# Optimization experiments

Hardware: AMD Instinct MI355X
Metric: run time of the kernel (lower is better)

The kernel has to match this reference:

```python
import jax, jax.numpy as jnp
import numpy as np

EPS = 1e-5
RADIUS = 3.0
NSAMPLE = 32


def _bn(x, g, b, axes):
    # BatchNorm (training-mode batch statistics) over given axes; channel is axis 1.
    m = jnp.mean(x, axis=axes, keepdims=True)
    v = jnp.var(x, axis=axes, keepdims=True)
    shape = [1, -1] + [1] * (x.ndim - 2)
    return (x - m) / jnp.sqrt(v + EPS) * g.reshape(shape) + b.reshape(shape)


def _ball_query(xyz, new_xyz, radius, nsample):
    # xyz: (B,N,3) support points, new_xyz: (B,M,3) query points -> idx (B,M,nsample) int32
    # Matches pointnet2 ball_query: first `nsample` points within radius (in index order),
    # padded with the first found index (0 if none found).
    d2 = (jnp.sum(new_xyz ** 2, -1)[:, :, None]
          + jnp.sum(xyz ** 2, -1)[:, None, :]
          - 2.0 * jnp.einsum('bmd,bnd->bmn', new_xyz, xyz))  # (B,M,N)
    mask = d2 < radius * radius
    N = xyz.shape[1]
    scores = jnp.where(mask, -jnp.arange(N, dtype=d2.dtype), -jnp.inf)
    vals, _ = jax.lax.top_k(scores, nsample)  # largest scores = smallest indices, in order
    valid = jnp.isfinite(vals)
    idx = jnp.where(valid, -vals, 0.0).astype(jnp.int32)
    first = idx[..., 0:1]
    return jnp.where(valid, idx, first)


def setup_inputs() -> dict:
    key = jax.random.key(0)
    ks = jax.random.split(key, 8)
    B, N, M, C = 4, 16384, 2048, 128
    inp = {
        'ffps_xyz': jax.random.normal(ks[0], (B, M, 3), jnp.float32),
        'backbone_xyz': jax.random.normal(ks[1], (B, N, 3), jnp.float32),
        'backbone_features': jax.random.normal(ks[2], (B, C, N), jnp.float32),
        'shift_w0': jax.random.normal(ks[3], (64, 3), jnp.float32) * 0.1,
        'shift_g0': jnp.ones((64,), jnp.float32),
        'shift_b0': jnp.zeros((64,), jnp.float32),
        'shift_w1': jax.random.normal(ks[4], (3, 64), jnp.float32) * 0.1,
        'shift_g1': jnp.ones((3,), jnp.float32),
        'shift_b1': jnp.zeros((3,), jnp.float32),
        'mlp_w0': jax.random.normal(ks[5], (128, 131), jnp.float32) * 0.05,
        'mlp_g0': jnp.ones((128,), jnp.float32),
        'mlp_b0': jnp.zeros((128,), jnp.float32),
        'mlp_w1': jax.random.normal(ks[6], (256, 128), jnp.float32) * 0.05,
        'mlp_g1': jnp.ones((256,), jnp.float32),
        'mlp_b1': jnp.zeros((256,), jnp.float32),
    }
    return inp


def reference(ffps_xyz, backbone_xyz, backbone_features,
              shift_w0, shift_g0, shift_b0, shift_w1, shift_g1, shift_b1,
              mlp_w0, mlp_g0, mlp_b0, mlp_w1, mlp_g1, mlp_b1):
    # shift_layer: Conv1d(1x1)+BN1d+ReLU stack on candidate coordinates
    q = ffps_xyz.transpose(0, 2, 1)  # (B,3,M)
    h = jax.nn.relu(_bn(jnp.einsum('oc,bcm->bom', shift_w0, q), shift_g0, shift_b0, (0, 2)))
    h = jax.nn.relu(_bn(jnp.einsum('oc,bcm->bom', shift_w1, h), shift_g1, shift_b1, (0, 2)))
    new_xyz = h.transpose(0, 2, 1)  # (B,M,3) shifted candidate centers

    # QueryAndGroup(use_xyz=True)
    idx = _ball_query(backbone_xyz, new_xyz, RADIUS, NSAMPLE)        # (B,M,K)
    grouped_xyz = jax.vmap(lambda x, i: x[i])(backbone_xyz, idx)      # (B,M,K,3)
    grouped_feat = jax.vmap(lambda f, i: f[:, i])(backbone_features, idx)  # (B,C,M,K)
    rel = (grouped_xyz - new_xyz[:, :, None, :]).transpose(0, 3, 1, 2)     # (B,3,M,K)
    g = jnp.concatenate([rel, grouped_feat], axis=1)                  # (B,3+C,M,K)

    # Conv2d(1x1)+BN2d+ReLU stack
    g = jax.nn.relu(_bn(jnp.einsum('oc,bcmk->bomk', mlp_w0, g), mlp_g0, mlp_b0, (0, 2, 3)))
    g = jax.nn.relu(_bn(jnp.einsum('oc,bcmk->bomk', mlp_w1, g), mlp_g1, mlp_b1, (0, 2, 3)))

    # max-pool over neighbor dim, squeeze, transpose -> (B,M,C_out)
    out = jnp.max(g, axis=3)  # (B,C_out,M)
    return out.transpose(0, 2, 1)
```

## Files before the change

### kernel.cpp

```cpp
#include <hip/hip_runtime.h>
#include <cstddef>
#include <cstdint>

#define B_ 4
#define N_ 16384
#define M_ 2048
#define C_ 128
#define NQ (B_*M_)
#define NSAMP 32
#define SAMP (NQ*NSAMP)
#define EPS_ 1e-5f
#define R2_ 9.0f

typedef short s8v  __attribute__((ext_vector_type(8)));
typedef short s4v  __attribute__((ext_vector_type(4)));
typedef float f32x4 __attribute__((ext_vector_type(4)));

#define ST_COPIES 8
#define ST_S0S 0
#define ST_S0Q 64
#define ST_S1S 128
#define ST_S1Q 136
#define ST_M1S 144
#define ST_M1Q 272
#define ST_M2S 400
#define ST_M2Q 656

__device__ __forceinline__ unsigned short f2bf(float f) {
    unsigned int u = __builtin_bit_cast(unsigned int, f);
    u += 0x7fffu + ((u >> 16) & 1u);
    return (unsigned short)(u >> 16);
}
__device__ __forceinline__ float bf2f(unsigned short h) {
    unsigned int u = ((unsigned int)h) << 16;
    return __builtin_bit_cast(float, u);
}

__global__ void k_prep_w(const float* __restrict__ w0, const float* __restrict__ w1,
                         unsigned short* __restrict__ w0p, unsigned short* __restrict__ w1p) {
    int i = blockIdx.x * 256 + threadIdx.x;
    const int tot0 = 128 * 160;
    if (i < tot0) {
        int o = i / 160, c = i - o * 160;
        float v = 0.f;
        if (c < 128)      v = w0[o * 131 + 3 + c];
        else if (c < 131) v = w0[o * 131 + (c - 128)];
        w0p[i] = f2bf(v);
    }
    int j = i - tot0;
    if (j >= 0 && j < 256 * 128) w1p[j] = f2bf(w1[j]);
}

__global__ void k_transpose(const float* __restrict__ feat, unsigned short* __restrict__ featT) {
    __shared__ unsigned short tl[64][130];
    int b  = blockIdx.x >> 8;
    int n0 = (blockIdx.x & 255) * 64;
    const float* src = feat + (size_t)b * C_ * N_;
    int t = threadIdx.x;
    for (int i = 0; i < 32; ++i) {
        int lin = i * 256 + t;
        int c = lin >> 6, n = lin & 63;
        tl[n][c] = f2bf(src[(size_t)c * N_ + n0 + n]);
    }
    __syncthreads();
    unsigned short* dst = featT + ((size_t)b * N_ + n0) * 128;
    #pragma unroll
    for (int i = 0; i < 4; ++i) {
        int lin = i * 256 + t;
        int n = lin >> 4, cg = lin & 15;
        s8v v;
        #pragma unroll
        for (int e = 0; e < 8; ++e) v[e] = (short)tl[n][cg*8 + e];
        *(s8v*)(dst + (size_t)n * 128 + cg * 8) = v;
    }
}

__global__ void k_shift0(const float* __restrict__ xyz, const float* __restrict__ w0s,
                         float* __restrict__ t0, float* __restrict__ stats) {
    __shared__ float w[192];
    __shared__ float ps[4][64], pq[4][64];
    int t = threadIdx.x, wave = t >> 6, lane = t & 63;
    if (t < 192) w[t] = w0s[t];
    __syncthreads();
    int p = blockIdx.x * 256 + t;
    float q0 = xyz[p*3], q1 = xyz[p*3+1], q2 = xyz[p*3+2];
    float* orow = t0 + (size_t)p * 64;
    #pragma unroll
    for (int o = 0; o < 64; ++o) {
        float v = w[3*o]*q0 + w[3*o+1]*q1 + w[3*o+2]*q2;
        orow[o] = v;
        float s = v, sq = v * v;
        #pragma unroll
        for (int mk = 32; mk; mk >>= 1) { s += __shfl_xor(s, mk); sq += __shfl_xor(sq, mk); }
        if (lane == 0) { ps[wave][o] = s; pq[wave][o] = sq; }
    }
    __syncthreads();
    if (t < 64) {
        float s = ps[0][t] + ps[1][t] + ps[2][t] + ps[3][t];
        float q = pq[0][t] + pq[1][t] + pq[2][t] + pq[3][t];
        atomicAdd(&stats[ST_S0S + t], s);
        atomicAdd(&stats[ST_S0Q + t], q);
    }
}

__global__ void k_shift1(const float* __restrict__ t0, const float* __restrict__ w1s,
                         const float* __restrict__ g0, const float* __restrict__ b0,
                         float* __restrict__ t1, float* __restrict__ stats) {
    __shared__ float aa[64], bb[64], wl[192];
    __shared__ float ps[4][3], pq[4][3];
    int t = threadIdx.x, wave = t >> 6, lane = t & 63;
    if (t < 64) {
        float mean = stats[ST_S0S + t] * (1.f / NQ);
        float var  = stats[ST_S0Q + t] * (1.f / NQ) - mean * mean;
        float a = g0[t] * rsqrtf(var + EPS_);
        aa[t] = a; bb[t] = b0[t] - mean * a;
    }
    if (t < 192) wl[t] = w1s[t];
    __syncthreads();
    int p = blockIdx.x * 256 + t;
    const f32x4* xr = (const f32x4*)(t0 + (size_t)p * 64);
    float v0 = 0.f, v1 = 0.f, v2 = 0.f;
    #pragma unroll
    for (int i = 0; i < 16; ++i) {
        f32x4 x = xr[i];
        #pragma unroll
        for (int j = 0; j < 4; ++j) {
            int c = 4*i + j;
            float h = fmaxf(0.f, aa[c] * x[j] + bb[c]);
            v0 += wl[c] * h; v1 += wl[64 + c] * h; v2 += wl[128 + c] * h;
        }
    }
    t1[p*3] = v0; t1[p*3+1] = v1; t1[p*3+2] = v2;
    float vv[3] = {v0, v1, v2};
    #pragma unroll
    for (int o = 0; o < 3; ++o) {
        float s = vv[o], q = vv[o] * vv[o];
        #pragma unroll
        for (int mk = 32; mk; mk >>= 1) { s += __shfl_xor(s, mk); q += __shfl_xor(q, mk); }
        if (lane == 0) { ps[wave][o] = s; pq[wave][o] = q; }
    }
    __syncthreads();
    if (t < 3) {
        float s = ps[0][t] + ps[1][t] + ps[2][t] + ps[3][t];
        float q = pq[0][t] + pq[1][t] + pq[2][t] + pq[3][t];
        atomicAdd(&stats[ST_S1S + t], s);
        atomicAdd(&stats[ST_S1Q + t], q);
    }
}

__global__ void k_shift2(const float* __restrict__ t1, const float* __restrict__ g1,
                         const float* __restrict__ b1, const float* __restrict__ stats,
                         float* __restrict__ nxyz) {
    int p = blockIdx.x * 256 + threadIdx.x;
    for (int o = 0; o < 3; ++o) {
        float mean = stats[ST_S1S + o] * (1.f / NQ);
        float var  = stats[ST_S1Q + o] * (1.f / NQ) - mean * mean;
        float a = g1[o] * rsqrtf(var + EPS_);
        float bbv = b1[o] - mean * a;
        nxyz[p*3+o] = fmaxf(0.f, a * t1[p*3+o] + bbv);
    }
}

__global__ void __launch_bounds__(256)
k_ballq(const float* __restrict__ bxyz, const float* __restrict__ nxyz,
        int* __restrict__ idxb) {
    __shared__ float pts[4096 * 3];
    int tid = threadIdx.x, wave = tid >> 6, lane = tid & 63;
    int b = blockIdx.x >> 5;
    int qbase = blockIdx.x * 64 + wave * 16;
    const float* bp = bxyz + (size_t)b * N_ * 3;
    unsigned long long below = (lane == 63) ? ~0ull >> 1 : ((1ull << lane) - 1ull);

    float qx[16], qy[16], qz[16], sq[16];
    int cnt[16], first[16];
    #pragma unroll
    for (int q = 0; q < 16; ++q) {
        qx[q] = nxyz[(qbase+q)*3]; qy[q] = nxyz[(qbase+q)*3+1]; qz[q] = nxyz[(qbase+q)*3+2];
        sq[q] = __fadd_rn(__fadd_rn(__fmul_rn(qx[q],qx[q]), __fmul_rn(qy[q],qy[q])), __fmul_rn(qz[q],qz[q]));
        cnt[q] = 0; first[q] = 0;
    }

    for (int ch = 0; ch < 4; ++ch) {
        __syncthreads();
        {
            const f32x4* src = (const f32x4*)(bp + ch * 12288);
            f32x4* d4 = (f32x4*)pts;
            #pragma unroll
            for (int i = 0; i < 12; ++i) d4[i*256 + tid] = src[i*256 + tid];
        }
        __syncthreads();
        #pragma unroll
        for (int q = 0; q < 16; ++q) {
            if (cnt[q] >= 32) continue;
            for (int j0 = 0; j0 < 4096 && cnt[q] < 32; j0 += 256) {
                #pragma unroll
                for (int u = 0; u < 4; ++u) {
                    if (cnt[q] < 32) {
                        int jl = j0 + u*64 + lane;
                        float x = pts[jl*3], y = pts[jl*3+1], z = pts[jl*3+2];
                        float sx  = __fadd_rn(__fadd_rn(__fmul_rn(x,x), __fmul_rn(y,y)), __fmul_rn(z,z));
                        float dot = __fadd_rn(__fadd_rn(__fmul_rn(qx[q],x), __fmul_rn(qy[q],y)), __fmul_rn(qz[q],z));
                        float d2  = __fsub_rn(__fadd_rn(sq[q], sx), __fmul_rn(2.0f, dot));
                        unsigned long long m = __ballot(d2 < R2_);
                        if (cnt[q] == 0 && m != 0ull)
                            first[q] = ch*4096 + j0 + u*64 + __ffsll((long long)m) - 1;
                        int pre = cnt[q] + __popcll(m & below);
                        if (((m >> lane) & 1ull) && pre < 32)
                            idxb[(size_t)(qbase+q)*32 + pre] = ch*4096 + jl;
                        cnt[q] += __popcll(m);
                    }
                }
            }
        }
    }
    #pragma unroll
    for (int q = 0; q < 16; ++q) {
        if (cnt[q] < 32) {
            int f = (cnt[q] == 0) ? 0 : first[q];
            for (int k = cnt[q] + lane; k < 32; k += 64) idxb[(size_t)(qbase+q)*32 + k] = f;
        }
    }
}

__global__ void __launch_bounds__(256)
k_gemm1(const unsigned short* __restrict__ featT, const float* __restrict__ bxyz,
        const float* __restrict__ nxyz, const int* __restrict__ idxb,
        const unsigned short* __restrict__ w0p, unsigned short* __restrict__ y1,
        float* __restrict__ stats) {
    __shared__ unsigned short gt[64][168];
    __shared__ int pidx[256];
    __shared__ float nq[8][3];
    int tid  = threadIdx.x;
    int wave = tid >> 6, lane = tid & 63, quad = lane >> 4, l16 = lane & 15;
    int s2 = tid >> 2, part4 = tid & 3;
    int b = blockIdx.x >> 8;
    float* stc = stats + (size_t)(blockIdx.x & (ST_COPIES-1)) * 1024;

    s8v bfr[2][5];
    #pragma unroll
    for (int g = 0; g < 2; ++g)
        #pragma unroll
        for (int kk = 0; kk < 5; ++kk)
            bfr[g][kk] = *(const s8v*)(w0p + (wave*32 + g*16 + l16)*160 + kk*32 + quad*8);

    pidx[tid] = idxb[blockIdx.x * 256 + tid];
    if (tid < 24) nq[tid / 3][tid % 3] = nxyz[blockIdx.x * 24 + tid];
    if (tid < 64)
        for (int c = 131; c < 160; ++c) gt[tid][c] = 0;
    __syncthreads();

    s8v pv[4]; float prel0 = 0.f, prel1 = 0.f, prel2 = 0.f;
    {
        int pp = pidx[s2];
        const unsigned short* src = featT + ((size_t)(b * N_ + pp)) * 128 + part4 * 32;
        pv[0] = *(const s8v*)src;        pv[1] = *(const s8v*)(src + 8);
        pv[2] = *(const s8v*)(src + 16); pv[3] = *(const s8v*)(src + 24);
        if (tid < 64) {
            int pq_ = pidx[tid];
            const float* bx = bxyz + (size_t)(b * N_ + pq_) * 3;
            int q = tid >> 5;
            prel0 = bx[0] - nq[q][0]; prel1 = bx[1] - nq[q][1]; prel2 = bx[2] - nq[q][2];
        }
    }
    float csum[2] = {}, csq[2] = {};

    for (int r = 0; r < 4; ++r) {
        __syncthreads();
        *(s8v*)&gt[s2][part4*32]      = pv[0];
        *(s8v*)&gt[s2][part4*32 + 8]  = pv[1];
        *(s8v*)&gt[s2][part4*32 + 16] = pv[2];
        *(s8v*)&gt[s2][part4*32 + 24] = pv[3];
        if (tid < 64) {
            gt[tid][128] = f2bf(prel0); gt[tid][129] = f2bf(prel1); gt[tid][130] = f2bf(prel2);
        }
        if (r + 1 < 4) {
            int pp = pidx[(r+1)*64 + s2];
            const unsigned short* src = featT + ((size_t)(b * N_ + pp)) * 128 + part4 * 32;
            pv[0] = *(const s8v*)src;        pv[1] = *(const s8v*)(src + 8);
            pv[2] = *(const s8v*)(src + 16); pv[3] = *(const s8v*)(src + 24);
            if (tid < 64) {
                int pq_ = pidx[(r+1)*64 + tid];
                const float* bx = bxyz + (size_t)(b * N_ + pq_) * 3;
                int q = (r+1)*2 + (tid >> 5);
                prel0 = bx[0] - nq[q][0]; prel1 = bx[1] - nq[q][1]; prel2 = bx[2] - nq[q][2];
            }
        }
        __syncthreads();
        f32x4 acc[2][4] = {};
        #pragma unroll
        for (int kk = 0; kk < 5; ++kk) {
            s8v at[4];
            #pragma unroll
            for (int t = 0; t < 4; ++t)
                at[t] = *(const s8v*)&gt[t*16 + l16][kk*32 + quad*8];
            #pragma unroll
            for (int g = 0; g < 2; ++g)
                #pragma unroll
                for (int t = 0; t < 4; ++t)
                    acc[g][t] = __builtin_amdgcn_mfma_f32_16x16x32_bf16(at[t], bfr[g][kk], acc[g][t], 0, 0, 0);
        }
        size_t sbase = (size_t)blockIdx.x * 256 + r * 64;
        #pragma unroll
        for (int g = 0; g < 2; ++g) {
            int ch = wave*32 + g*16 + l16;
            #pragma unroll
            for (int t = 0; t < 4; ++t)
                #pragma unroll
                for (int rr = 0; rr < 4; ++rr) {
                    float v = acc[g][t][rr];
                    y1[(sbase + t*16 + quad*4 + rr) * 128 + ch] = f2bf(v);
                    csum[g] += v; csq[g] += v * v;
                }
        }
    }
    #pragma unroll
    for (int g = 0; g < 2; ++g) {
        float s = csum[g], q = csq[g];
        s += __shfl_xor(s, 16); s += __shfl_xor(s, 32);
        q += __shfl_xor(q, 16); q += __shfl_xor(q, 32);
        if (quad == 0) {
            int ch = wave*32 + g*16 + l16;
            atomicAdd(&stc[ST_M1S + ch], s);
            atomicAdd(&stc[ST_M1Q + ch], q);
        }
    }
}

__global__ void __launch_bounds__(256)
k_gemm2(const unsigned short* __restrict__ y1, const unsigned short* __restrict__ w1p,
        const float* __restrict__ g1m, const float* __restrict__ b1m,
        float* __restrict__ stats, float* __restrict__ mx, float* __restrict__ mn) {
    __shared__ unsigned short ht[256][136];
    __shared__ float a1l[128], b1l[128];
    int tid = threadIdx.x;
    float* stc = stats + (size_t)(blockIdx.x & (ST_COPIES-1)) * 1024;
    if (tid < 128) {
        float ssum = 0.f, ssq = 0.f;
        #pragma unroll
        for (int c8 = 0; c8 < ST_COPIES; ++c8) {
            ssum += stats[c8*1024 + ST_M1S + tid];
            ssq  += stats[c8*1024 + ST_M1Q + tid];
        }
        float mean = ssum * (1.f / SAMP);
        float var  = ssq  * (1.f / SAMP) - mean * mean;
        float a = g1m[tid] * rsqrtf(var + EPS_);
        a1l[tid] = a; b1l[tid] = b1m[tid] - mean * a;
    }
    __syncthreads();
    int wave = tid >> 6, lane = tid & 63, quad = lane >> 4, l16 = lane & 15;
    int s = tid >> 3, part = tid & 7;

    float a1r[16], b1r[16];
    {
        const float* ap = &a1l[part * 16];
        const float* bp = &b1l[part * 16];
        #pragma unroll
        for (int i = 0; i < 16; ++i) { a1r[i] = ap[i]; b1r[i] = bp[i]; }
    }
    s8v bfr[4][4];
    #pragma unroll
    for (int g = 0; g < 4; ++g)
        #pragma unroll
        for (int kk = 0; kk < 4; ++kk)
            bfr[g][kk] = *(const s8v*)(w1p + (wave*64 + g*16 + l16)*128 + kk*32 + quad*8);

    size_t base = (size_t)blockIdx.x * 256;
    s8v rv[8][2];
    #pragma unroll
    for (int q = 0; q < 8; ++q) {
        const unsigned short* src = y1 + (base + q*32 + s) * 128 + part * 16;
        rv[q][0] = *(const s8v*)src; rv[q][1] = *(const s8v*)(src + 8);
    }
    #pragma unroll
    for (int q = 0; q < 8; ++q) {
        s8v o0, o1;
        #pragma unroll
        for (int e = 0; e < 8; ++e) {
            float f0 = bf2f((unsigned short)rv[q][0][e]);
            float f1 = bf2f((unsigned short)rv[q][1][e]);
            o0[e] = (short)f2bf(fmaxf(0.f, a1r[e]     * f0 + b1r[e]));
            o1[e] = (short)f2bf(fmaxf(0.f, a1r[8 + e] * f1 + b1r[8 + e]));
        }
        *(s8v*)&ht[q*32 + s][part*16]     = o0;
        *(s8v*)&ht[q*32 + s][part*16 + 8] = o1;
    }
    __syncthreads();

    float csum[4] = {}, csq[4] = {};
    for (int r = 0; r < 4; ++r) {
        f32x4 acc[4][4] = {};
        #pragma unroll
        for (int kk = 0; kk < 4; ++kk) {
            s8v at[4];
            #pragma unroll
            for (int t = 0; t < 4; ++t)
                at[t] = *(const s8v*)&ht[r*64 + t*16 + l16][kk*32 + quad*8];
            #pragma unroll
            for (int g = 0; g < 4; ++g)
                #pragma unroll
                for (int t = 0; t < 4; ++t)
                    acc[g][t] = __builtin_amdgcn_mfma_f32_16x16x32_bf16(at[t], bfr[g][kk], acc[g][t], 0, 0, 0);
        }
        #pragma unroll
        for (int g = 0; g < 4; ++g) {
            float sacc = 0.f, qacc = 0.f;
            #pragma unroll
            for (int t = 0; t < 4; ++t)
                #pragma unroll
                for (int e = 0; e < 4; ++e) {
                    float v = acc[g][t][e];
                    sacc += v; qacc = __builtin_fmaf(v, v, qacc);
                }
            csum[g] += sacc; csq[g] += qacc;
            #pragma unroll
            for (int qh = 0; qh < 2; ++qh) {
                int gq = blockIdx.x * 8 + r*2 + qh;
                f32x4 v0 = acc[g][2*qh], v1 = acc[g][2*qh + 1];
                float hi = fmaxf(fmaxf(fmaxf(v0[0], v0[1]), fmaxf(v0[2], v0[3])),
                                 fmaxf(fmaxf(v1[0], v1[1]), fmaxf(v1[2], v1[3])));
                float lo = fminf(fminf(fminf(v0[0], v0[1]), fminf(v0[2], v0[3])),
                                 fminf(fminf(v1[0], v1[1]), fminf(v1[2], v1[3])));
                hi = fmaxf(hi, __shfl_xor(hi, 16)); hi = fmaxf(hi, __shfl_xor(hi, 32));
                lo = fminf(lo, __shfl_xor(lo, 16)); lo = fminf(lo, __shfl_xor(lo, 32));
                if (quad == 0) {
                    int c = wave*64 + g*16 + l16;
                    mx[(size_t)gq * 256 + c] = hi;
                    mn[(size_t)gq * 256 + c] = lo;
                }
            }
        }
    }
    #pragma unroll
    for (int g = 0; g < 4; ++g) {
        float sv = csum[g], q = csq[g];
        sv += __shfl_xor(sv, 16); sv += __shfl_xor(sv, 32);
        q  += __shfl_xor(q, 16);  q  += __shfl_xor(q, 32);
        if (quad == 0) {
            int c = wave*64 + g*16 + l16;
            atomicAdd(&stc[ST_M2S + c], sv);
            atomicAdd(&stc[ST_M2Q + c], q);
        }
    }
}

__global__ void k_bn2(const float* __restrict__ g2m, const float* __restrict__ b2m,
                      const float* __restrict__ stats, float* __restrict__ ab2) {
    int c = threadIdx.x;
    float ssum = 0.f, ssq = 0.f;
    #pragma unroll
    for (int c8 = 0; c8 < ST_COPIES; ++c8) {
        ssum += stats[c8*1024 + ST_M2S + c];
        ssq  += stats[c8*1024 + ST_M2Q + c];
    }
    float mean = ssum * (1.f / SAMP);
    float var  = ssq  * (1.f / SAMP) - mean * mean;
    float a = g2m[c] * rsqrtf(var + EPS_);
    ab2[c] = a; ab2[256 + c] = b2m[c] - mean * a;
}

__global__ void k_final(const float* __restrict__ mx, const float* __restrict__ mn,
                        const float* __restrict__ ab2, float* __restrict__ out) {
    int i = blockIdx.x * 256 + threadIdx.x;
    int c = i & 255;
    float a = ab2[c], bb = ab2[256 + c];
    float v = (a >= 0.f) ? mx[i] : mn[i];
    out[i] = fmaxf(0.f, a * v + bb);
}

extern "C" void kernel_launch(void* const* d_in, const int* in_sizes, int n_in,
                              void* d_out, int out_size, void* d_ws, size_t ws_size,
                              hipStream_t stream) {
    const float* ffps = (const float*)d_in[0];
    const float* bxyz = (const float*)d_in[1];
    const float* feat = (const float*)d_in[2];
    const float* sw0  = (const float*)d_in[3];
    const float* sg0  = (const float*)d_in[4];
    const float* sb0  = (const float*)d_in[5];
    const float* sw1  = (const float*)d_in[6];
    const float* sg1  = (const float*)d_in[7];
    const float* sb1  = (const float*)d_in[8];
    const float* mw0  = (const float*)d_in[9];
    const float* mg0  = (const float*)d_in[10];
    const float* mb0  = (const float*)d_in[11];
    const float* mw1  = (const float*)d_in[12];
    const float* mg1  = (const float*)d_in[13];
    const float* mb1  = (const float*)d_in[14];
    float* out = (float*)d_out;

    char* ws = (char*)d_ws;
    size_t off = 0;
    auto alloc = [&](size_t bytes) -> void* {
        void* p = ws + off;
        off += (bytes + 255) & ~(size_t)255;
        return p;
    };
    float*          stats = (float*)alloc(ST_COPIES * 1024 * 4);
    float*          t0    = (float*)alloc((size_t)NQ * 64 * 4);
    float*          t1    = (float*)alloc((size_t)NQ * 3 * 4);
    float*          nxyz  = (float*)alloc((size_t)NQ * 3 * 4);
    int*            idxb  = (int*)alloc((size_t)NQ * 32 * 4);
    unsigned short* w0p   = (unsigned short*)alloc(128 * 160 * 2);
    unsigned short* w1p   = (unsigned short*)alloc(256 * 128 * 2);
    unsigned short* featT = (unsigned short*)alloc((size_t)B_ * N_ * 128 * 2);
    unsigned short* y1    = (unsigned short*)alloc((size_t)SAMP * 128 * 2);
    float*          mx    = (float*)alloc((size_t)NQ * 256 * 4);
    float*          mn    = (float*)alloc((size_t)NQ * 256 * 4);
    float*          ab2   = (float*)alloc(512 * 4);
    (void)in_sizes; (void)n_in; (void)out_size; (void)ws_size;

    hipMemsetAsync(stats, 0, ST_COPIES * 1024 * 4, stream);
    k_prep_w   <<<208, 256, 0, stream>>>(mw0, mw1, w0p, w1p);
    k_transpose<<<B_ * 256, 256, 0, stream>>>(feat, featT);
    k_shift0   <<<NQ / 256, 256, 0, stream>>>(ffps, sw0, t0, stats);
    k_shift1   <<<NQ / 256, 256, 0, stream>>>(t0, sw1, sg0, sb0, t1, stats);
    k_shift2   <<<NQ / 256, 256, 0, stream>>>(t1, sg1, sb1, stats, nxyz);
    k_ballq    <<<NQ / 64, 256, 0, stream>>>(bxyz, nxyz, idxb);
    k_gemm1    <<<NQ / 8, 256, 0, stream>>>(featT, bxyz, nxyz, idxb, w0p, y1, stats);
    k_gemm2    <<<NQ / 8, 256, 0, stream>>>(y1, w1p, mg0, mb0, stats, mx, mn);
    k_bn2      <<<1, 256, 0, stream>>>(mg1, mb1, stats, ab2);
    k_final    <<<NQ, 256, 0, stream>>>(mx, mn, ab2, out);
}
```

Measured before the change: 250.6 us.

## Fold shift2 into ball query, store one sign-selected max, widen stats copies

The final shift BN+ReLU is computed directly inside the ball-query kernel, which also writes nxyz, so one launch and one round trip through memory go away. gemm2 now uses the sign of gamma from the second MLP BN, which sets the sign of the BN scale, to keep only the needed extreme of max or min. It does this with a sign-bit XOR, so one buffer is written instead of two and k_final reads half as much. The number of replicated stats accumulators is doubled to spread atomic contention, at the cost of more reduction reads.

```diff
diff --git a/kernel.cpp b/kernel.cpp
--- a/kernel.cpp
+++ b/kernel.cpp
@@ -16,7 +16,7 @@
 typedef short s4v  __attribute__((ext_vector_type(4)));
 typedef float f32x4 __attribute__((ext_vector_type(4)));
 
-#define ST_COPIES 8
+#define ST_COPIES 16
 #define ST_S0S 0
 #define ST_S0Q 64
 #define ST_S1S 128
@@ -34,6 +34,9 @@
 __device__ __forceinline__ float bf2f(unsigned short h) {
     unsigned int u = ((unsigned int)h) << 16;
     return __builtin_bit_cast(float, u);
+}
+__device__ __forceinline__ float fxor(float f, unsigned m) {
+    return __builtin_bit_cast(float, __builtin_bit_cast(unsigned, f) ^ m);
 }
 
 __global__ void k_prep_w(const float* __restrict__ w0, const float* __restrict__ w1,
@@ -148,21 +151,10 @@
     }
 }
 
-__global__ void k_shift2(const float* __restrict__ t1, const float* __restrict__ g1,
-                         const float* __restrict__ b1, const float* __restrict__ stats,
-                         float* __restrict__ nxyz) {
-    int p = blockIdx.x * 256 + threadIdx.x;
-    for (int o = 0; o < 3; ++o) {
-        float mean = stats[ST_S1S + o] * (1.f / NQ);
-        float var  = stats[ST_S1Q + o] * (1.f / NQ) - mean * mean;
-        float a = g1[o] * rsqrtf(var + EPS_);
-        float bbv = b1[o] - mean * a;
-        nxyz[p*3+o] = fmaxf(0.f, a * t1[p*3+o] + bbv);
-    }
-}
-
 __global__ void __launch_bounds__(256)
-k_ballq(const float* __restrict__ bxyz, const float* __restrict__ nxyz,
+k_ballq(const float* __restrict__ bxyz, const float* __restrict__ t1,
+        const float* __restrict__ g1, const float* __restrict__ b1,
+        const float* __restrict__ stats, float* __restrict__ nxyz,
         int* __restrict__ idxb) {
     __shared__ float pts[4096 * 3];
     int tid = threadIdx.x, wave = tid >> 6, lane = tid & 63;
@@ -171,13 +163,29 @@
     const float* bp = bxyz + (size_t)b * N_ * 3;
     unsigned long long below = (lane == 63) ? ~0ull >> 1 : ((1ull << lane) - 1ull);
 
+    float av[3], bv[3];
+    #pragma unroll
+    for (int o = 0; o < 3; ++o) {
+        float mean = stats[ST_S1S + o] * (1.f / NQ);
+        float var  = stats[ST_S1Q + o] * (1.f / NQ) - mean * mean;
+        float a = g1[o] * rsqrtf(var + EPS_);
+        av[o] = a; bv[o] = b1[o] - mean * a;
+    }
     float qx[16], qy[16], qz[16], sq[16];
     int cnt[16], first[16];
     #pragma unroll
     for (int q = 0; q < 16; ++q) {
-        qx[q] = nxyz[(qbase+q)*3]; qy[q] = nxyz[(qbase+q)*3+1]; qz[q] = nxyz[(qbase+q)*3+2];
+        qx[q] = fmaxf(0.f, av[0] * t1[(qbase+q)*3]   + bv[0]);
+        qy[q] = fmaxf(0.f, av[1] * t1[(qbase+q)*3+1] + bv[1]);
+        qz[q] = fmaxf(0.f, av[2] * t1[(qbase+q)*3+2] + bv[2]);
         sq[q] = __fadd_rn(__fadd_rn(__fmul_rn(qx[q],qx[q]), __fmul_rn(qy[q],qy[q])), __fmul_rn(qz[q],qz[q]));
         cnt[q] = 0; first[q] = 0;
+    }
+    if (lane < 48) {
+        int q = lane / 3, o = lane % 3;
+        float ao = (o == 0) ? av[0] : ((o == 1) ? av[1] : av[2]);
+        float bo = (o == 0) ? bv[0] : ((o == 1) ? bv[1] : bv[2]);
+        nxyz[(qbase+q)*3 + o] = fmaxf(0.f, ao * t1[(qbase+q)*3 + o] + bo);
     }
 
     for (int ch = 0; ch < 4; ++ch) {
@@ -329,7 +337,8 @@
 __global__ void __launch_bounds__(256)
 k_gemm2(const unsigned short* __restrict__ y1, const unsigned short* __restrict__ w1p,
         const float* __restrict__ g1m, const float* __restrict__ b1m,
-        float* __restrict__ stats, float* __restrict__ mx, float* __restrict__ mn) {
+        const float* __restrict__ g2m,
+        float* __restrict__ stats, float* __restrict__ mv) {
     __shared__ unsigned short ht[256][136];
     __shared__ float a1l[128], b1l[128];
     int tid = threadIdx.x;
@@ -358,11 +367,15 @@
         for (int i = 0; i < 16; ++i) { a1r[i] = ap[i]; b1r[i] = bp[i]; }
     }
     s8v bfr[4][4];
-    #pragma unroll
-    for (int g = 0; g < 4; ++g)
+    unsigned fmask[4];
+    #pragma unroll
+    for (int g = 0; g < 4; ++g) {
+        int c = wave*64 + g*16 + l16;
+        fmask[g] = (g2m[c] >= 0.f) ? 0u : 0x80000000u;
         #pragma unroll
         for (int kk = 0; kk < 4; ++kk)
-            bfr[g][kk] = *(const s8v*)(w1p + (wave*64 + g*16 + l16)*128 + kk*32 + quad*8);
+            bfr[g][kk] = *(const s8v*)(w1p + c*128 + kk*32 + quad*8);
+    }
 
     size_t base = (size_t)blockIdx.x * 256;
     s8v rv[8][2];
@@ -416,16 +429,16 @@
             for (int qh = 0; qh < 2; ++qh) {
                 int gq = blockIdx.x * 8 + r*2 + qh;
                 f32x4 v0 = acc[g][2*qh], v1 = acc[g][2*qh + 1];
-                float hi = fmaxf(fmaxf(fmaxf(v0[0], v0[1]), fmaxf(v0[2], v0[3])),
-                                 fmaxf(fmaxf(v1[0], v1[1]), fmaxf(v1[2], v1[3])));
-                float lo = fminf(fminf(fminf(v0[0], v0[1]), fminf(v0[2], v0[3])),
-                                 fminf(fminf(v1[0], v1[1]), fminf(v1[2], v1[3])));
-                hi = fmaxf(hi, __shfl_xor(hi, 16)); hi = fmaxf(hi, __shfl_xor(hi, 32));
-                lo = fminf(lo, __shfl_xor(lo, 16)); lo = fminf(lo, __shfl_xor(lo, 32));
+                float m = fxor(v0[0], fmask[g]);
+                #pragma unroll
+                for (int e = 1; e < 4; ++e) m = fmaxf(m, fxor(v0[e], fmask[g]));
+                #pragma unroll
+                for (int e = 0; e < 4; ++e) m = fmaxf(m, fxor(v1[e], fmask[g]));
+                m = fmaxf(m, __shfl_xor(m, 16));
+                m = fmaxf(m, __shfl_xor(m, 32));
                 if (quad == 0) {
                     int c = wave*64 + g*16 + l16;
-                    mx[(size_t)gq * 256 + c] = hi;
-                    mn[(size_t)gq * 256 + c] = lo;
+                    mv[(size_t)gq * 256 + c] = fxor(m, fmask[g]);
                 }
             }
         }
@@ -458,13 +471,11 @@
     ab2[c] = a; ab2[256 + c] = b2m[c] - mean * a;
 }
 
-__global__ void k_final(const float* __restrict__ mx, const float* __restrict__ mn,
-                        const float* __restrict__ ab2, float* __restrict__ out) {
+__global__ void k_final(const float* __restrict__ mv, const float* __restrict__ ab2,
+                        float* __restrict__ out) {
     int i = blockIdx.x * 256 + threadIdx.x;
     int c = i & 255;
-    float a = ab2[c], bb = ab2[256 + c];
-    float v = (a >= 0.f) ? mx[i] : mn[i];
-    out[i] = fmaxf(0.f, a * v + bb);
+    out[i] = fmaxf(0.f, ab2[c] * mv[i] + ab2[256 + c]);
 }
 
 extern "C" void kernel_launch(void* const* d_in, const int* in_sizes, int n_in,
@@ -503,8 +514,7 @@
     unsigned short* w1p   = (unsigned short*)alloc(256 * 128 * 2);
     unsigned short* featT = (unsigned short*)alloc((size_t)B_ * N_ * 128 * 2);
     unsigned short* y1    = (unsigned short*)alloc((size_t)SAMP * 128 * 2);
-    float*          mx    = (float*)alloc((size_t)NQ * 256 * 4);
-    float*          mn    = (float*)alloc((size_t)NQ * 256 * 4);
+    float*          mv    = (float*)alloc((size_t)NQ * 256 * 4);
     float*          ab2   = (float*)alloc(512 * 4);
     (void)in_sizes; (void)n_in; (void)out_size; (void)ws_size;
 
@@ -513,10 +523,9 @@
     k_transpose<<<B_ * 256, 256, 0, stream>>>(feat, featT);
     k_shift0   <<<NQ / 256, 256, 0, stream>>>(ffps, sw0, t0, stats);
     k_shift1   <<<NQ / 256, 256, 0, stream>>>(t0, sw1, sg0, sb0, t1, stats);
-    k_shift2   <<<NQ / 256, 256, 0, stream>>>(t1, sg1, sb1, stats, nxyz);
-    k_ballq    <<<NQ / 64, 256, 0, stream>>>(bxyz, nxyz, idxb);
+    k_ballq    <<<NQ / 64, 256, 0, stream>>>(bxyz, t1, sg1, sb1, stats, nxyz, idxb);
     k_gemm1    <<<NQ / 8, 256, 0, stream>>>(featT, bxyz, nxyz, idxb, w0p, y1, stats);
-    k_gemm2    <<<NQ / 8, 256, 0, stream>>>(y1, w1p, mg0, mb0, stats, mx, mn);
+    k_gemm2    <<<NQ / 8, 256, 0, stream>>>(y1, w1p, mg0, mb0, mg1, stats, mv);
     k_bn2      <<<1, 256, 0, stream>>>(mg1, mb1, stats, ab2);
-    k_final    <<<NQ, 256, 0, stream>>>(mx, mn, ab2, out);
-}
+    k_final    <<<NQ, 256, 0, stream>>>(mv, ab2, out);
+}
```

Result: no change. 245.8 us (-1.9%).
